# Performance work log

Hardware: AMD Instinct MI355X
Metric: run time of the kernel (lower is better)

Reference implementation:

```python
import jax, jax.numpy as jnp
import numpy as np

B, S, D = 1, 2048, 2048
H, KV, HD = 16, 2, 128        # heads, kv heads, head_dim
Q_SIZE, KV_SIZE = H * HD, KV * HD
NEG = -1e9


def setup_inputs() -> dict:
    key = jax.random.key(0)
    ks = jax.random.split(key, 5)
    hidden_states = jax.random.normal(ks[0], (B, S, D), dtype=jnp.float32)
    # rotary tables (Gemma/Qwen style: theta=10000, half-dim frequencies)
    inv_freq = 1.0 / (10000.0 ** (jnp.arange(0, HD, 2, dtype=jnp.float32) / HD))  # [HD/2]
    angles = jnp.arange(S, dtype=jnp.float32)[:, None] * inv_freq[None, :]        # [S, HD/2]
    freqs_cos = jnp.cos(angles)
    freqs_sin = jnp.sin(angles)
    kv_write_indices = jnp.arange(S, dtype=jnp.int32)
    k_cache = jnp.zeros((B, S, KV, HD), dtype=jnp.float32)
    v_cache = jnp.zeros((B, S, KV, HD), dtype=jnp.float32)
    causal = jnp.tril(jnp.ones((S, S), dtype=bool))
    mask = jnp.where(causal, 0.0, NEG).astype(jnp.float32)[None, None]  # [1,1,S,S]
    W_qkv = jax.random.normal(ks[1], (D, Q_SIZE + 2 * KV_SIZE), dtype=jnp.float32) * (D ** -0.5)
    b_qkv = jax.random.normal(ks[2], (Q_SIZE + 2 * KV_SIZE,), dtype=jnp.float32) * 0.02
    W_o = jax.random.normal(ks[3], (Q_SIZE, D), dtype=jnp.float32) * (Q_SIZE ** -0.5)
    return {
        "hidden_states": hidden_states, "freqs_cos": freqs_cos, "freqs_sin": freqs_sin,
        "kv_write_indices": kv_write_indices, "k_cache": k_cache, "v_cache": v_cache,
        "mask": mask, "W_qkv": W_qkv, "b_qkv": b_qkv, "W_o": W_o,
    }


def _rope(x, cos, sin):
    # x: [B, S, h, HD]; cos/sin: [S, HD/2]. Half-split (Gemma complex) layout.
    x1, x2 = jnp.split(x, 2, axis=-1)
    c = cos[None, :, None, :]
    s = sin[None, :, None, :]
    return jnp.concatenate([x1 * c - x2 * s, x1 * s + x2 * c], axis=-1)


def reference(hidden_states, freqs_cos, freqs_sin, kv_write_indices,
              k_cache, v_cache, mask, W_qkv, b_qkv, W_o):
    b, s, _ = hidden_states.shape
    qkv = hidden_states @ W_qkv + b_qkv                       # [B,S,(H+2KV)*HD]
    xq, xk, xv = jnp.split(qkv, [Q_SIZE, Q_SIZE + KV_SIZE], axis=-1)
    xq = xq.reshape(b, s, H, HD)
    xk = xk.reshape(b, s, KV, HD)
    xv = xv.reshape(b, s, KV, HD)
    xq = _rope(xq, freqs_cos, freqs_sin)
    xk = _rope(xk, freqs_cos, freqs_sin)
    # KV-cache write (index_copy_ along seq dim)
    key = k_cache.at[:, kv_write_indices].set(xk)             # [B,T,KV,HD]
    value = v_cache.at[:, kv_write_indices].set(xv)
    # GQA: repeat_interleave kv heads to H
    nrep = H // KV
    key = jnp.repeat(key, nrep, axis=2)                       # [B,T,H,HD]
    value = jnp.repeat(value, nrep, axis=2)
    q = jnp.transpose(xq, (0, 2, 1, 3)) * (HD ** -0.5)        # [B,H,S,HD]
    k = jnp.transpose(key, (0, 2, 1, 3))                      # [B,H,T,HD]
    v = jnp.transpose(value, (0, 2, 1, 3))
    scores = jnp.einsum("bhqd,bhkd->bhqk", q, k) + mask       # [B,H,S,T]
    probs = jax.nn.softmax(scores, axis=-1)
    out = jnp.einsum("bhqk,bhkd->bhqd", probs, v)             # [B,H,S,HD]
    out = jnp.transpose(out, (0, 2, 1, 3)).reshape(b, s, Q_SIZE)
    return out @ W_o                                          # [B,S,D]
```

## Files before the change

kernel.cpp:

```cpp
#include <hip/hip_runtime.h>
#include <hip/hip_bf16.h>

#define S_LEN 2048
#define D_MODEL 2048
#define NH 16
#define NKV 2
#define HD 128
#define QKV_N 2560
#define Q_SCALE_L2E (0.08838834764831845f * 1.4426950408889634f)

#define EPP 192

typedef short short8 __attribute__((ext_vector_type(8)));
typedef short s16x4 __attribute__((ext_vector_type(4)));
typedef float f32x4 __attribute__((ext_vector_type(4)));
using u16 = unsigned short;

struct PartTab {
  int ent[EPP];
  int rpStart[64];
  int rpN[64];
  constexpr PartTab() : ent{}, rpStart{}, rpN{} {
    int T[64] = {}, n[64] = {};
    int S = 0;
    for (int rp = 0; rp < 64; ++rp) {
      T[rp] = (rp + 2) >> 1;
      n[rp] = (T[rp] + 5) / 6;
      S += n[rp];
    }
    while (S > EPP) {
      int best = -1, bc = 1 << 30;
      for (int rp = 0; rp < 64; ++rp)
        if (n[rp] > 1) {
          int c = (T[rp] + n[rp] - 2) / (n[rp] - 1);
          if (c < bc) { bc = c; best = rp; }
        }
      --n[best]; --S;
    }
    int e = 0;
    for (int rp = 0; rp < 64; ++rp) {
      rpStart[rp] = e;
      rpN[rp] = n[rp];
      for (int c = 0; c < n[rp]; ++c) {
        int tlo = c * T[rp] / n[rp];
        int thi = (c + 1) * T[rp] / n[rp];
        ent[e++] = rp | (tlo << 6) | ((thi - tlo) << 12) | ((n[rp] == 1) ? (1 << 18) : 0);
      }
    }
  }
};
__constant__ PartTab d_tab = PartTab();

__device__ inline u16 f2b(float x) {
  __hip_bfloat16 h = __float2bfloat16(x);
  return *(u16*)&h;
}
__device__ inline float b2f(u16 x) {
  __hip_bfloat16 h = *(__hip_bfloat16*)&x;
  return __bfloat162float(h);
}
__device__ inline bool is_f32(const unsigned int* fc) {
  return (fc[0] & 0xFFFFu) == 0u;
}
__device__ inline u16 ld_cvt(const void* p, size_t i, bool f32) {
  return f32 ? f2b(((const float*)p)[i]) : ((const u16*)p)[i];
}

__device__ inline void async_copy16(const u16* g, u16* l) {
  __builtin_amdgcn_global_load_lds(
      (const __attribute__((address_space(1))) unsigned int*)g,
      (__attribute__((address_space(3))) unsigned int*)l, 16, 0, 0);
}

__global__ void convert_k(const void* __restrict__ in, u16* __restrict__ out,
                          int n, const unsigned int* __restrict__ fc) {
  const bool f32 = is_f32(fc);
  int i = blockIdx.x * 256 + threadIdx.x;
  if (i < n) out[i] = ld_cvt(in, i, f32);
}

__global__ void prep_k(const void* __restrict__ fcos, const void* __restrict__ fsin,
                       const void* __restrict__ bqkv, u16* __restrict__ cCos,
                       u16* __restrict__ cSin, u16* __restrict__ cBias) {
  const bool f32 = is_f32((const unsigned int*)fcos);
  int i = blockIdx.x * 256 + threadIdx.x;
  if (i < 131072)       cCos[i] = ld_cvt(fcos, i, f32);
  else if (i < 262144)  cSin[i - 131072] = ld_cvt(fsin, i - 131072, f32);
  else if (i < 264704)  cBias[i - 262144] = ld_cvt(bqkv, i - 262144, f32);
}

__global__ void transpose_k(const void* __restrict__ in, u16* __restrict__ out,
                            int R, int C, const unsigned int* __restrict__ fc) {
  __shared__ u16 tile[64][65];
  const bool f32 = is_f32(fc);
  const int t = threadIdx.x;
  const int r0 = blockIdx.y * 64, c0 = blockIdx.x * 64;
  for (int i = 0; i < 16; ++i) {
    int idx = i * 256 + t;
    int r = idx >> 6, c = idx & 63;
    tile[r][c] = ld_cvt(in, (size_t)(r0 + r) * C + c0 + c, f32);
  }
  __syncthreads();
  for (int i = 0; i < 16; ++i) {
    int idx = i * 256 + t;
    int r = idx >> 6, c = idx & 63;
    out[(size_t)(c0 + r) * R + r0 + c] = tile[c][r];
  }
}

template<int M, int N, int K, int KS>
__global__ __launch_bounds__(256, 2) void gemm_splitk(const u16* __restrict__ A,
                                                      const u16* __restrict__ BT,
                                                      u16* __restrict__ P0,
                                                      u16* __restrict__ P1) {
  __shared__ __align__(16) u16 lA[16 * 64 * 8];
  __shared__ __align__(16) u16 lB[16 * 64 * 8];
  const int t = threadIdx.x, lane = t & 63, w = t >> 6;
  const int wr = w & 1, wc = w >> 1;
  const int m0 = blockIdx.y * 128, n0 = blockIdx.x * 128;
  const int koff = blockIdx.z * KS;
  const int l15 = lane & 15, quad = lane >> 4;
  const int swz = (quad * 16 + (l15 ^ quad)) * 8;

  int srcoff[4], sdst[4];
  for (int qq = 0; qq < 4; ++qq) {
    int f = qq * 256 + t;
    int row = f >> 3, kc = f & 7;
    int j = kc >> 2, q4 = kc & 3, tile = row >> 4, lr = row & 15;
    sdst[qq] = ((j * 8 + tile) * 64 + q4 * 16 + (lr ^ q4)) * 8;
    srcoff[qq] = row * K + kc * 8;
  }

  f32x4 acc[4][4] = {};
  for (int k0 = koff; k0 < koff + KS; k0 += 64) {
    short8 av[4], bv[4];
    for (int qq = 0; qq < 4; ++qq) {
      av[qq] = *(const short8*)&A [(size_t)m0 * K + k0 + srcoff[qq]];
      bv[qq] = *(const short8*)&BT[(size_t)n0 * K + k0 + srcoff[qq]];
    }
    __syncthreads();
    for (int qq = 0; qq < 4; ++qq) {
      *(short8*)&lA[sdst[qq]] = av[qq];
      *(short8*)&lB[sdst[qq]] = bv[qq];
    }
    __syncthreads();
    for (int j = 0; j < 2; ++j) {
      short8 af[4], bf[4];
      for (int i = 0; i < 4; ++i)
        af[i] = *(const short8*)&lA[(j * 8 + wr * 4 + i) * 512 + swz];
      for (int jj = 0; jj < 4; ++jj)
        bf[jj] = *(const short8*)&lB[(j * 8 + wc * 4 + jj) * 512 + swz];
      for (int i = 0; i < 4; ++i)
        for (int jj = 0; jj < 4; ++jj)
          acc[i][jj] = __builtin_amdgcn_mfma_f32_16x16x32_bf16(af[i], bf[jj],
                                                               acc[i][jj], 0, 0, 0);
    }
  }

  u16* P = blockIdx.z ? P1 : P0;
  for (int i = 0; i < 4; ++i)
    for (int jj = 0; jj < 4; ++jj) {
      int row = m0 + wr * 64 + i * 16 + quad * 4;
      int col = n0 + wc * 64 + jj * 16 + l15;
      for (int r = 0; r < 4; ++r)
        P[(size_t)(row + r) * N + col] = f2b(acc[i][jj][r]);
    }
}


__global__ void rope_k(const u16* __restrict__ P0, const u16* __restrict__ P1,
                       const u16* __restrict__ bias, const u16* __restrict__ cosT,
                       const u16* __restrict__ sinT, const int* __restrict__ idx,
                       u16* __restrict__ q, u16* __restrict__ kfrag) {
  const int s = blockIdx.y;
  const int c = blockIdx.x * 256 + threadIdx.x;
  const bool isq = c < 2048;
  int d, colbase;
  if (isq) { d = c & 127; colbase = c & ~127; }
  else     { int c2 = c - 2048; d = c2 & 127; colbase = 2048 + (c2 & ~127); }
  const int dd = d & 63;
  const size_t b1 = (size_t)s * QKV_N + colbase + dd;
  float x1 = b2f(P0[b1]) + b2f(P1[b1]) + b2f(bias[colbase + dd]);
  float x2 = b2f(P0[b1 + 64]) + b2f(P1[b1 + 64]) + b2f(bias[colbase + dd + 64]);
  float cv = b2f(cosT[s * 64 + dd]);
  float sv = b2f(sinT[s * 64 + dd]);
  float v = (d < 64) ? (x1 * cv - x2 * sv) : (x1 * sv + x2 * cv);
  if (isq) {
    q[(size_t)s * D_MODEL + c] = f2b(v * Q_SCALE_L2E);
  } else {
    int c2 = c - 2048;
    int kvh = c2 >> 7, dcol = c2 & 127;
    int srow = idx[s];
    int sblk = srow >> 6, ns = (srow >> 4) & 3, lr = srow & 15;
    int cc = dcol >> 5, qd = (dcol >> 3) & 3, j = dcol & 7;
    kfrag[kvh * 262144 + sblk * 8192 + ((ns * 4 + cc) * 64 + qd * 16 + lr) * 8 + j] = f2b(v);
  }
}

__global__ void vscat_k(const u16* __restrict__ P0, const u16* __restrict__ P1,
                        const u16* __restrict__ bias, const int* __restrict__ idx,
                        u16* __restrict__ vfrag) {
  int id = blockIdx.x * 256 + threadIdx.x;
  int s = id >> 8, cv = id & 255;
  int kvh = cv >> 7, dcol = cv & 127;
  const size_t gi = (size_t)s * QKV_N + 2304 + cv;
  float v = b2f(P0[gi]) + b2f(P1[gi]) + b2f(bias[2304 + cv]);
  int srow = idx[s];
  int sblk = srow >> 6, kvl = srow & 63;
  int c2 = kvl >> 5, qd = (kvl >> 2) & 3, j = ((kvl >> 4) & 1) * 4 + (kvl & 3);
  int d = dcol >> 4, lr = dcol & 15;
  vfrag[kvh * 262144 + sblk * 8192 + ((c2 * 8 + d) * 64 + qd * 16 + lr) * 8 + j] = f2b(v);
}

__global__ void reduce_out_k(const u16* __restrict__ G0, const u16* __restrict__ G1,
                             void* __restrict__ out, const unsigned int* __restrict__ fc) {
  const bool f32 = is_f32(fc);
  int i = blockIdx.x * 256 + threadIdx.x;
  float v = b2f(G0[i]) + b2f(G1[i]);
  if (f32) ((float*)out)[i] = v;
  else     ((u16*)out)[i] = f2b(v);
}

__global__ __launch_bounds__(256, 3) void attn_part_k(const u16* __restrict__ Q,
                                                      const u16* __restrict__ Kf,
                                                      const u16* __restrict__ Vf,
                                                      u16* __restrict__ attnOut,
                                                      u16* __restrict__ pO_A,
                                                      u16* __restrict__ pO_B,
                                                      float* __restrict__ ml) {
  __shared__ __align__(16) u16 sm[16384];
  const int t = threadIdx.x, lane = t & 63, w = t >> 6;
  const int l15 = lane & 15, quad = lane >> 4;

  const int b = blockIdx.x;
  const int plane = b / EPP;
  const int ent = d_tab.ent[b - plane * EPP];
  const int rp = ent & 63, tlo = (ent >> 6) & 63, nkb = (ent >> 12) & 63;
  const bool direct = (ent >> 18) & 1;
  const int kvh = plane >> 1, hh = plane & 1;
  const int h = kvh * 8 + hh * 4 + w;
  const int qrow0 = rp * 32;
  const int kv_lo = tlo * 64;
  const int gw = b * 4 + w;

  const u16* Kb = Kf + kvh * 262144;
  const u16* Vb = Vf + kvh * 262144;

  short8 aq[2][4];
  for (int ss = 0; ss < 2; ++ss)
    for (int cc = 0; cc < 4; ++cc)
      aq[ss][cc] = *(const short8*)&Q[(size_t)(qrow0 + ss * 16 + l15) * D_MODEL
                                      + h * HD + cc * 32 + quad * 8];

  f32x4 oacc[2][8] = {};
  float m_i[2] = {-1e30f, -1e30f}, l_i[2] = {0.0f, 0.0f};

  {
    const u16* kt = Kb + (size_t)(kv_lo >> 6) * 8192;
    const u16* vt = Vb + (size_t)(kv_lo >> 6) * 8192;
    for (int f = 0; f < 4; ++f) {
      int fr = w * 4 + f;
      async_copy16(kt + fr * 512 + lane * 8, &sm[fr * 512]);
      async_copy16(vt + fr * 512 + lane * 8, &sm[8192 + fr * 512]);
    }
  }
  __syncthreads();

  for (int kb = 0; kb < nkb; ++kb) {
    const int kv0 = kv_lo + kb * 64;
    f32x4 st[2][4] = {};
    __builtin_amdgcn_s_setprio(1);
    for (int ns = 0; ns < 4; ++ns) {
      short8 bk[4];
      for (int cc = 0; cc < 4; ++cc)
        bk[cc] = *(const short8*)&sm[((ns * 4 + cc) * 64 + lane) * 8];
      for (int ss = 0; ss < 2; ++ss)
        for (int cc = 0; cc < 4; ++cc)
          st[ss][ns] = __builtin_amdgcn_mfma_f32_16x16x32_bf16(bk[cc], aq[ss][cc],
                                                               st[ss][ns], 0, 0, 0);
    }
    __builtin_amdgcn_s_setprio(0);
    __syncthreads();
    if (kb + 1 < nkb) {
      const u16* kt = Kb + (size_t)((kv0 + 64) >> 6) * 8192;
      for (int f = 0; f < 4; ++f) {
        int fr = w * 4 + f;
        async_copy16(kt + fr * 512 + lane * 8, &sm[fr * 512]);
      }
    }
    const bool need_mask = (kv0 + 63) > qrow0;
    short8 pb[2][2];
    for (int ss = 0; ss < 2; ++ss) {
      float mb = -1e30f;
      if (need_mask) {
        int qg = qrow0 + ss * 16 + l15;
        #pragma unroll
        for (int ns = 0; ns < 4; ++ns) {
          int kvg = kv0 + ns * 16 + quad * 4;
          #pragma unroll
          for (int rr = 0; rr < 4; ++rr) {
            float s = (kvg + rr <= qg) ? st[ss][ns][rr] : -1e30f;
            st[ss][ns][rr] = s;
            mb = fmaxf(mb, s);
          }
        }
      } else {
        #pragma unroll
        for (int ns = 0; ns < 4; ++ns)
          #pragma unroll
          for (int rr = 0; rr < 4; ++rr) mb = fmaxf(mb, st[ss][ns][rr]);
      }
      mb = fmaxf(mb, __shfl_xor(mb, 16, 64));
      mb = fmaxf(mb, __shfl_xor(mb, 32, 64));
      if (!__all(mb <= m_i[ss] + 8.0f)) {
        float mn = fmaxf(m_i[ss], mb);
        float alpha = exp2f(m_i[ss] - mn);
        m_i[ss] = mn;
        l_i[ss] *= alpha;
        #pragma unroll
        for (int dt = 0; dt < 8; ++dt) oacc[ss][dt] *= alpha;
      }
      float rs = 0.0f;
      #pragma unroll
      for (int ns = 0; ns < 4; ++ns)
        #pragma unroll
        for (int rr = 0; rr < 4; ++rr) {
          float e = exp2f(st[ss][ns][rr] - m_i[ss]);
          rs += e;
          pb[ss][ns >> 1][(ns & 1) * 4 + rr] = (short)f2b(e);
        }
      rs += __shfl_xor(rs, 16, 64);
      rs += __shfl_xor(rs, 32, 64);
      l_i[ss] += rs;
    }
    __builtin_amdgcn_s_setprio(1);
    for (int c2 = 0; c2 < 2; ++c2)
      for (int dt = 0; dt < 8; ++dt) {
        short8 av = *(const short8*)&sm[8192 + ((c2 * 8 + dt) * 64 + lane) * 8];
        for (int ss = 0; ss < 2; ++ss)
          oacc[ss][dt] = __builtin_amdgcn_mfma_f32_16x16x32_bf16(av, pb[ss][c2],
                                                                 oacc[ss][dt], 0, 0, 0);
      }
    __builtin_amdgcn_s_setprio(0);
    if (kb + 1 < nkb) {
      __syncthreads();
      const u16* vt = Vb + (size_t)((kv0 + 64) >> 6) * 8192;
      for (int f = 0; f < 4; ++f) {
        int fr = w * 4 + f;
        async_copy16(vt + fr * 512 + lane * 8, &sm[8192 + fr * 512]);
      }
    }
  }

  __syncthreads();
  u16* Ow = &sm[w * 2176];
  const int er = lane >> 2, ec = lane & 3;
  for (int ss = 0; ss < 2; ++ss) {
    float inv = direct ? (1.0f / l_i[ss]) : 1.0f;
    for (int dt = 0; dt < 8; ++dt) {
      s16x4 pk;
      for (int rr = 0; rr < 4; ++rr) pk[rr] = (short)f2b(oacc[ss][dt][rr] * inv);
      *(s16x4*)&Ow[l15 * 136 + dt * 16 + quad * 4] = pk;
    }
    __builtin_amdgcn_s_waitcnt(0xC07F);
    short8 o0 = *(const short8*)&Ow[er * 136 + ec * 32];
    short8 o1 = *(const short8*)&Ow[er * 136 + ec * 32 + 8];
    short8 o2 = *(const short8*)&Ow[er * 136 + ec * 32 + 16];
    short8 o3 = *(const short8*)&Ow[er * 136 + ec * 32 + 24];
    __builtin_amdgcn_s_waitcnt(0xC07F);
    if (direct) {
      size_t ga = (size_t)(qrow0 + ss * 16 + er) * D_MODEL + h * HD + ec * 32;
      *(short8*)&attnOut[ga]      = o0;
      *(short8*)&attnOut[ga + 8]  = o1;
      *(short8*)&attnOut[ga + 16] = o2;
      *(short8*)&attnOut[ga + 24] = o3;
    } else {
      u16* po = (gw < 2048) ? (pO_A + (size_t)gw * 4096)
                            : (pO_B + (size_t)(gw - 2048) * 4096);
      int ra = (ss * 16 + er) * 128 + ec * 32;
      *(short8*)&po[ra]      = o0;
      *(short8*)&po[ra + 8]  = o1;
      *(short8*)&po[ra + 16] = o2;
      *(short8*)&po[ra + 24] = o3;
      if (quad == 0) {
        ml[gw * 64 + (ss * 16 + l15) * 2]     = m_i[ss];
        ml[gw * 64 + (ss * 16 + l15) * 2 + 1] = l_i[ss];
      }
    }
  }
}

__global__ void attn_combine_k(const u16* __restrict__ pO_A,
                               const u16* __restrict__ pO_B,
                               const float* __restrict__ ml,
                               u16* __restrict__ attn) {
  const int h = blockIdx.x >> 6, rp = blockIdx.x & 63;
  const int nch = d_tab.rpN[rp];
  if (nch == 1) return;
  const int start = d_tab.rpStart[rp];
  const int t = threadIdx.x;
  const int row = t >> 3;
  const int dblk = t & 7;
  const int plane = (h >> 3) * 2 + ((h >> 2) & 1);
  const int w = h & 3;

  int gws[8];
  float wt[8];
  float mx = -1e30f;
  for (int c = 0; c < nch; ++c) {
    gws[c] = (plane * EPP + start + c) * 4 + w;
    mx = fmaxf(mx, ml[gws[c] * 64 + row * 2]);
  }
  float lsum = 0.0f;
  for (int c = 0; c < nch; ++c) {
    float m = ml[gws[c] * 64 + row * 2];
    float l = ml[gws[c] * 64 + row * 2 + 1];
    wt[c] = exp2f(m - mx);
    lsum += l * wt[c];
  }
  float inv = 1.0f / lsum;

  float acc[16];
  #pragma unroll
  for (int j = 0; j < 16; ++j) acc[j] = 0.0f;
  const int poff = row * 128 + dblk * 16;
  for (int c = 0; c < nch; ++c) {
    const u16* po = (gws[c] < 2048) ? (pO_A + (size_t)gws[c] * 4096)
                                    : (pO_B + (size_t)(gws[c] - 2048) * 4096);
    short8 lo = *(const short8*)&po[poff];
    short8 hi = *(const short8*)&po[poff + 8];
    float wc = wt[c];
    #pragma unroll
    for (int j = 0; j < 8; ++j) acc[j]     += b2f((u16)lo[j]) * wc;
    #pragma unroll
    for (int j = 0; j < 8; ++j) acc[8 + j] += b2f((u16)hi[j]) * wc;
  }
  short8 o0, o1;
  #pragma unroll
  for (int j = 0; j < 8; ++j) o0[j] = (short)f2b(acc[j] * inv);
  #pragma unroll
  for (int j = 0; j < 8; ++j) o1[j] = (short)f2b(acc[8 + j] * inv);
  const size_t orow = (size_t)(rp * 32 + row) * D_MODEL + h * HD + dblk * 16;
  *(short8*)&attn[orow]     = o0;
  *(short8*)&attn[orow + 8] = o1;
}

extern "C" void kernel_launch(void* const* d_in, const int* in_sizes, int n_in,
                              void* d_out, int out_size, void* d_ws, size_t ws_size,
                              hipStream_t stream) {
  const void* hidden = d_in[0];
  const void* fcos   = d_in[1];
  const void* fsin   = d_in[2];
  const int* idx     = (const int*)d_in[3];
  u16* maskScratch   = (u16*)d_in[6];
  const void* Wqkv = d_in[7];
  const void* bqkv = d_in[8];
  const void* Wo   = d_in[9];
  const unsigned int* fc = (const unsigned int*)fcos;

  u16* ws = (u16*)d_ws;
  u16* cHid   = ws;
  u16* cCos   = ws + 4194304;
  u16* cSin   = ws + 4325376;
  u16* cBias  = ws + 4456448;
  u16* WqkvT  = ws + 4461056;
  u16* q      = WqkvT;
  u16* G1     = WqkvT;
  u16* P0     = ws + 9703936;
  u16* attn   = P0;
  u16* P1     = ws + 14946816;
  u16* pO_B   = P1;
  float* ml   = (float*)(P1 + 4194304);
  u16* WoT    = ws + 20189696;
  u16* kfrag  = ws;
  u16* vfrag  = ws + 524288;
  u16* G0     = ws;

  convert_k<<<(4194304 + 255) / 256, 256, 0, stream>>>(hidden, cHid, 4194304, fc);
  prep_k<<<(264704 + 255) / 256, 256, 0, stream>>>(fcos, fsin, bqkv, cCos, cSin, cBias);
  transpose_k<<<dim3(40, 32), 256, 0, stream>>>(Wqkv, WqkvT, D_MODEL, QKV_N, fc);
  transpose_k<<<dim3(32, 32), 256, 0, stream>>>(Wo, WoT, D_MODEL, D_MODEL, fc);
  gemm_splitk<S_LEN, QKV_N, D_MODEL, D_MODEL / 2>
      <<<dim3(QKV_N / 128, S_LEN / 128, 2), 256, 0, stream>>>(cHid, WqkvT, P0, P1);
  rope_k<<<dim3(9, S_LEN), 256, 0, stream>>>(P0, P1, cBias, cCos, cSin, idx, q, kfrag);
  vscat_k<<<2048, 256, 0, stream>>>(P0, P1, cBias, idx, vfrag);
  attn_part_k<<<4 * EPP, 256, 0, stream>>>(q, kfrag, vfrag, attn, maskScratch, pO_B, ml);
  attn_combine_k<<<16 * 64, 256, 0, stream>>>(maskScratch, pO_B, ml, attn);
  gemm_splitk<S_LEN, D_MODEL, D_MODEL, D_MODEL / 2>
      <<<dim3(D_MODEL / 128, S_LEN / 128, 2), 256, 0, stream>>>(attn, WoT, G0, G1);
  reduce_out_k<<<4194304 / 256, 256, 0, stream>>>(G0, G1, d_out, fc);
}
```

Before: 260.2 us.

## Vectorize elementwise kernels, fuse rope with V scatter, double-buffer attention K/V

Converts the convert, prep, transpose and reduce kernels to 8- or 4-wide vector loads and stores, replacing per-element accesses. Merges the rope and V-scatter kernels into one launch, with each rope thread now computing both halves of a rotation pair. Double-buffers K and V tiles in LDS within the attention kernel, prefetching the next block at the top of each iteration and dropping one barrier per step. The larger LDS footprint lowers the launch bound from 3 to 2 blocks per CU, which may reduce occupancy.

```diff
diff --git a/kernel.cpp b/kernel.cpp
--- a/kernel.cpp
+++ b/kernel.cpp
@@ -65,6 +65,19 @@
 __device__ inline u16 ld_cvt(const void* p, size_t i, bool f32) {
   return f32 ? f2b(((const float*)p)[i]) : ((const u16*)p)[i];
 }
+__device__ inline short8 ld8_cvt(const void* p, size_t i8, bool f32) {
+  short8 o;
+  if (f32) {
+    const float* f = (const float*)p + i8 * 8;
+    f32x4 a = *(const f32x4*)f;
+    f32x4 b = *(const f32x4*)(f + 4);
+    #pragma unroll
+    for (int j = 0; j < 4; ++j) { o[j] = (short)f2b(a[j]); o[4 + j] = (short)f2b(b[j]); }
+  } else {
+    o = *(const short8*)((const u16*)p + i8 * 8);
+  }
+  return o;
+}
 
 __device__ inline void async_copy16(const u16* g, u16* l) {
   __builtin_amdgcn_global_load_lds(
@@ -73,10 +86,10 @@
 }
 
 __global__ void convert_k(const void* __restrict__ in, u16* __restrict__ out,
-                          int n, const unsigned int* __restrict__ fc) {
+                          int n8, const unsigned int* __restrict__ fc) {
   const bool f32 = is_f32(fc);
   int i = blockIdx.x * 256 + threadIdx.x;
-  if (i < n) out[i] = ld_cvt(in, i, f32);
+  if (i < n8) *(short8*)&out[(size_t)i * 8] = ld8_cvt(in, i, f32);
 }
 
 __global__ void prep_k(const void* __restrict__ fcos, const void* __restrict__ fsin,
@@ -84,9 +97,9 @@
                        u16* __restrict__ cSin, u16* __restrict__ cBias) {
   const bool f32 = is_f32((const unsigned int*)fcos);
   int i = blockIdx.x * 256 + threadIdx.x;
-  if (i < 131072)       cCos[i] = ld_cvt(fcos, i, f32);
-  else if (i < 262144)  cSin[i - 131072] = ld_cvt(fsin, i - 131072, f32);
-  else if (i < 264704)  cBias[i - 262144] = ld_cvt(bqkv, i - 262144, f32);
+  if (i < 16384)       *(short8*)&cCos[(size_t)i * 8] = ld8_cvt(fcos, i, f32);
+  else if (i < 32768)  *(short8*)&cSin[(size_t)(i - 16384) * 8] = ld8_cvt(fsin, i - 16384, f32);
+  else if (i < 33088)  *(short8*)&cBias[(size_t)(i - 32768) * 8] = ld8_cvt(bqkv, i - 32768, f32);
 }
 
 __global__ void transpose_k(const void* __restrict__ in, u16* __restrict__ out,
@@ -95,16 +108,27 @@
   const bool f32 = is_f32(fc);
   const int t = threadIdx.x;
   const int r0 = blockIdx.y * 64, c0 = blockIdx.x * 64;
-  for (int i = 0; i < 16; ++i) {
-    int idx = i * 256 + t;
+  for (int i = 0; i < 4; ++i) {
+    int idx = (i * 256 + t) * 4;
     int r = idx >> 6, c = idx & 63;
-    tile[r][c] = ld_cvt(in, (size_t)(r0 + r) * C + c0 + c, f32);
+    if (f32) {
+      f32x4 v = *(const f32x4*)&((const float*)in)[(size_t)(r0 + r) * C + c0 + c];
+      #pragma unroll
+      for (int j = 0; j < 4; ++j) tile[r][c + j] = f2b(v[j]);
+    } else {
+      s16x4 v = *(const s16x4*)&((const u16*)in)[(size_t)(r0 + r) * C + c0 + c];
+      #pragma unroll
+      for (int j = 0; j < 4; ++j) tile[r][c + j] = (u16)v[j];
+    }
   }
   __syncthreads();
-  for (int i = 0; i < 16; ++i) {
-    int idx = i * 256 + t;
+  for (int i = 0; i < 4; ++i) {
+    int idx = (i * 256 + t) * 4;
     int r = idx >> 6, c = idx & 63;
-    out[(size_t)(c0 + r) * R + r0 + c] = tile[c][r];
+    s16x4 o;
+    #pragma unroll
+    for (int j = 0; j < 4; ++j) o[j] = (short)tile[c + j][r];
+    *(s16x4*)&out[(size_t)(c0 + r) * R + r0 + c] = o;
   }
 }
 
@@ -168,67 +192,82 @@
 }
 
 
-__global__ void rope_k(const u16* __restrict__ P0, const u16* __restrict__ P1,
-                       const u16* __restrict__ bias, const u16* __restrict__ cosT,
-                       const u16* __restrict__ sinT, const int* __restrict__ idx,
-                       u16* __restrict__ q, u16* __restrict__ kfrag) {
+__global__ void ropev_k(const u16* __restrict__ P0, const u16* __restrict__ P1,
+                        const u16* __restrict__ bias, const u16* __restrict__ cosT,
+                        const u16* __restrict__ sinT, const int* __restrict__ idx,
+                        u16* __restrict__ q, u16* __restrict__ kfrag,
+                        u16* __restrict__ vfrag) {
   const int s = blockIdx.y;
-  const int c = blockIdx.x * 256 + threadIdx.x;
-  const bool isq = c < 2048;
-  int d, colbase;
-  if (isq) { d = c & 127; colbase = c & ~127; }
-  else     { int c2 = c - 2048; d = c2 & 127; colbase = 2048 + (c2 & ~127); }
-  const int dd = d & 63;
-  const size_t b1 = (size_t)s * QKV_N + colbase + dd;
-  float x1 = b2f(P0[b1]) + b2f(P1[b1]) + b2f(bias[colbase + dd]);
-  float x2 = b2f(P0[b1 + 64]) + b2f(P1[b1 + 64]) + b2f(bias[colbase + dd + 64]);
-  float cv = b2f(cosT[s * 64 + dd]);
-  float sv = b2f(sinT[s * 64 + dd]);
-  float v = (d < 64) ? (x1 * cv - x2 * sv) : (x1 * sv + x2 * cv);
-  if (isq) {
-    q[(size_t)s * D_MODEL + c] = f2b(v * Q_SCALE_L2E);
+  const int id = blockIdx.x * 256 + threadIdx.x;
+  if (id >= 1408) return;
+  if (id < 1152) {
+    const int colbase = (id < 1024) ? (id >> 6) * 128
+                                    : 2048 + ((id - 1024) >> 6) * 128;
+    const int dd = id & 63;
+    const size_t b1 = (size_t)s * QKV_N + colbase + dd;
+    float x1 = b2f(P0[b1]) + b2f(P1[b1]) + b2f(bias[colbase + dd]);
+    float x2 = b2f(P0[b1 + 64]) + b2f(P1[b1 + 64]) + b2f(bias[colbase + dd + 64]);
+    float cv = b2f(cosT[s * 64 + dd]);
+    float sv = b2f(sinT[s * 64 + dd]);
+    float o1 = x1 * cv - x2 * sv;
+    float o2 = x1 * sv + x2 * cv;
+    if (id < 1024) {
+      q[(size_t)s * D_MODEL + colbase + dd]      = f2b(o1 * Q_SCALE_L2E);
+      q[(size_t)s * D_MODEL + colbase + dd + 64] = f2b(o2 * Q_SCALE_L2E);
+    } else {
+      int kvh = (colbase - 2048) >> 7;
+      int srow = idx[s];
+      int sblk = srow >> 6, ns = (srow >> 4) & 3, lr = srow & 15;
+      int cc1 = dd >> 5, qd1 = (dd >> 3) & 3, j1 = dd & 7;
+      kfrag[kvh * 262144 + sblk * 8192 + ((ns * 4 + cc1) * 64 + qd1 * 16 + lr) * 8 + j1] = f2b(o1);
+      int d2 = dd + 64;
+      int cc2 = d2 >> 5, qd2 = (d2 >> 3) & 3, j2 = d2 & 7;
+      kfrag[kvh * 262144 + sblk * 8192 + ((ns * 4 + cc2) * 64 + qd2 * 16 + lr) * 8 + j2] = f2b(o2);
+    }
   } else {
-    int c2 = c - 2048;
-    int kvh = c2 >> 7, dcol = c2 & 127;
+    const int cv_ = id - 1152;
+    const int kvh = cv_ >> 7, dcol = cv_ & 127;
+    const size_t gi = (size_t)s * QKV_N + 2304 + cv_;
+    float v = b2f(P0[gi]) + b2f(P1[gi]) + b2f(bias[2304 + cv_]);
     int srow = idx[s];
-    int sblk = srow >> 6, ns = (srow >> 4) & 3, lr = srow & 15;
-    int cc = dcol >> 5, qd = (dcol >> 3) & 3, j = dcol & 7;
-    kfrag[kvh * 262144 + sblk * 8192 + ((ns * 4 + cc) * 64 + qd * 16 + lr) * 8 + j] = f2b(v);
-  }
-}
-
-__global__ void vscat_k(const u16* __restrict__ P0, const u16* __restrict__ P1,
-                        const u16* __restrict__ bias, const int* __restrict__ idx,
-                        u16* __restrict__ vfrag) {
-  int id = blockIdx.x * 256 + threadIdx.x;
-  int s = id >> 8, cv = id & 255;
-  int kvh = cv >> 7, dcol = cv & 127;
-  const size_t gi = (size_t)s * QKV_N + 2304 + cv;
-  float v = b2f(P0[gi]) + b2f(P1[gi]) + b2f(bias[2304 + cv]);
-  int srow = idx[s];
-  int sblk = srow >> 6, kvl = srow & 63;
-  int c2 = kvl >> 5, qd = (kvl >> 2) & 3, j = ((kvl >> 4) & 1) * 4 + (kvl & 3);
-  int d = dcol >> 4, lr = dcol & 15;
-  vfrag[kvh * 262144 + sblk * 8192 + ((c2 * 8 + d) * 64 + qd * 16 + lr) * 8 + j] = f2b(v);
+    int sblk = srow >> 6, kvl = srow & 63;
+    int c2 = kvl >> 5, qd = (kvl >> 2) & 3, j = ((kvl >> 4) & 1) * 4 + (kvl & 3);
+    int d = dcol >> 4, lr = dcol & 15;
+    vfrag[kvh * 262144 + sblk * 8192 + ((c2 * 8 + d) * 64 + qd * 16 + lr) * 8 + j] = f2b(v);
+  }
 }
 
 __global__ void reduce_out_k(const u16* __restrict__ G0, const u16* __restrict__ G1,
                              void* __restrict__ out, const unsigned int* __restrict__ fc) {
   const bool f32 = is_f32(fc);
   int i = blockIdx.x * 256 + threadIdx.x;
-  float v = b2f(G0[i]) + b2f(G1[i]);
-  if (f32) ((float*)out)[i] = v;
-  else     ((u16*)out)[i] = f2b(v);
-}
-
-__global__ __launch_bounds__(256, 3) void attn_part_k(const u16* __restrict__ Q,
+  short8 a = *(const short8*)&G0[(size_t)i * 8];
+  short8 b = *(const short8*)&G1[(size_t)i * 8];
+  if (f32) {
+    f32x4 lo, hi;
+    #pragma unroll
+    for (int j = 0; j < 4; ++j) {
+      lo[j] = b2f((u16)a[j]) + b2f((u16)b[j]);
+      hi[j] = b2f((u16)a[4 + j]) + b2f((u16)b[4 + j]);
+    }
+    ((f32x4*)out)[(size_t)i * 2]     = lo;
+    ((f32x4*)out)[(size_t)i * 2 + 1] = hi;
+  } else {
+    short8 o;
+    #pragma unroll
+    for (int j = 0; j < 8; ++j) o[j] = (short)f2b(b2f((u16)a[j]) + b2f((u16)b[j]));
+    ((short8*)out)[i] = o;
+  }
+}
+
+__global__ __launch_bounds__(256, 2) void attn_part_k(const u16* __restrict__ Q,
                                                       const u16* __restrict__ Kf,
                                                       const u16* __restrict__ Vf,
                                                       u16* __restrict__ attnOut,
                                                       u16* __restrict__ pO_A,
                                                       u16* __restrict__ pO_B,
                                                       float* __restrict__ ml) {
-  __shared__ __align__(16) u16 sm[16384];
+  __shared__ __align__(16) u16 sm[32768];
   const int t = threadIdx.x, lane = t & 63, w = t >> 6;
   const int l15 = lane & 15, quad = lane >> 4;
 
@@ -268,26 +307,29 @@
 
   for (int kb = 0; kb < nkb; ++kb) {
     const int kv0 = kv_lo + kb * 64;
+    const int cur = (kb & 1) * 16384;
+    const int nxt = cur ^ 16384;
+    if (kb + 1 < nkb) {
+      const u16* kt = Kb + (size_t)((kv0 + 64) >> 6) * 8192;
+      const u16* vt = Vb + (size_t)((kv0 + 64) >> 6) * 8192;
+      for (int f = 0; f < 4; ++f) {
+        int fr = w * 4 + f;
+        async_copy16(kt + fr * 512 + lane * 8, &sm[nxt + fr * 512]);
+        async_copy16(vt + fr * 512 + lane * 8, &sm[nxt + 8192 + fr * 512]);
+      }
+    }
     f32x4 st[2][4] = {};
     __builtin_amdgcn_s_setprio(1);
     for (int ns = 0; ns < 4; ++ns) {
       short8 bk[4];
       for (int cc = 0; cc < 4; ++cc)
-        bk[cc] = *(const short8*)&sm[((ns * 4 + cc) * 64 + lane) * 8];
+        bk[cc] = *(const short8*)&sm[cur + ((ns * 4 + cc) * 64 + lane) * 8];
       for (int ss = 0; ss < 2; ++ss)
         for (int cc = 0; cc < 4; ++cc)
           st[ss][ns] = __builtin_amdgcn_mfma_f32_16x16x32_bf16(bk[cc], aq[ss][cc],
                                                                st[ss][ns], 0, 0, 0);
     }
     __builtin_amdgcn_s_setprio(0);
-    __syncthreads();
-    if (kb + 1 < nkb) {
-      const u16* kt = Kb + (size_t)((kv0 + 64) >> 6) * 8192;
-      for (int f = 0; f < 4; ++f) {
-        int fr = w * 4 + f;
-        async_copy16(kt + fr * 512 + lane * 8, &sm[fr * 512]);
-      }
-    }
     const bool need_mask = (kv0 + 63) > qrow0;
     short8 pb[2][2];
     for (int ss = 0; ss < 2; ++ss) {
@@ -336,23 +378,15 @@
     __builtin_amdgcn_s_setprio(1);
     for (int c2 = 0; c2 < 2; ++c2)
       for (int dt = 0; dt < 8; ++dt) {
-        short8 av = *(const short8*)&sm[8192 + ((c2 * 8 + dt) * 64 + lane) * 8];
+        short8 av = *(const short8*)&sm[cur + 8192 + ((c2 * 8 + dt) * 64 + lane) * 8];
         for (int ss = 0; ss < 2; ++ss)
           oacc[ss][dt] = __builtin_amdgcn_mfma_f32_16x16x32_bf16(av, pb[ss][c2],
                                                                  oacc[ss][dt], 0, 0, 0);
       }
     __builtin_amdgcn_s_setprio(0);
-    if (kb + 1 < nkb) {
-      __syncthreads();
-      const u16* vt = Vb + (size_t)((kv0 + 64) >> 6) * 8192;
-      for (int f = 0; f < 4; ++f) {
-        int fr = w * 4 + f;
-        async_copy16(vt + fr * 512 + lane * 8, &sm[8192 + fr * 512]);
-      }
-    }
-  }
-
-  __syncthreads();
+    __syncthreads();
+  }
+
   u16* Ow = &sm[w * 2176];
   const int er = lane >> 2, ec = lane & 3;
   for (int ss = 0; ss < 2; ++ss) {
@@ -476,17 +510,16 @@
   u16* vfrag  = ws + 524288;
   u16* G0     = ws;
 
-  convert_k<<<(4194304 + 255) / 256, 256, 0, stream>>>(hidden, cHid, 4194304, fc);
-  prep_k<<<(264704 + 255) / 256, 256, 0, stream>>>(fcos, fsin, bqkv, cCos, cSin, cBias);
+  convert_k<<<2048, 256, 0, stream>>>(hidden, cHid, 524288, fc);
+  prep_k<<<130, 256, 0, stream>>>(fcos, fsin, bqkv, cCos, cSin, cBias);
   transpose_k<<<dim3(40, 32), 256, 0, stream>>>(Wqkv, WqkvT, D_MODEL, QKV_N, fc);
   transpose_k<<<dim3(32, 32), 256, 0, stream>>>(Wo, WoT, D_MODEL, D_MODEL, fc);
   gemm_splitk<S_LEN, QKV_N, D_MODEL, D_MODEL / 2>
       <<<dim3(QKV_N / 128, S_LEN / 128, 2), 256, 0, stream>>>(cHid, WqkvT, P0, P1);
-  rope_k<<<dim3(9, S_LEN), 256, 0, stream>>>(P0, P1, cBias, cCos, cSin, idx, q, kfrag);
-  vscat_k<<<2048, 256, 0, stream>>>(P0, P1, cBias, idx, vfrag);
+  ropev_k<<<dim3(6, S_LEN), 256, 0, stream>>>(P0, P1, cBias, cCos, cSin, idx, q, kfrag, vfrag);
   attn_part_k<<<4 * EPP, 256, 0, stream>>>(q, kfrag, vfrag, attn, maskScratch, pO_B, ml);
   attn_combine_k<<<16 * 64, 256, 0, stream>>>(maskScratch, pO_B, ml, attn);
   gemm_splitk<S_LEN, D_MODEL, D_MODEL, D_MODEL / 2>
       <<<dim3(D_MODEL / 128, S_LEN / 128, 2), 256, 0, stream>>>(attn, WoT, G0, G1);
-  reduce_out_k<<<4194304 / 256, 256, 0, stream>>>(G0, G1, d_out, fc);
-}
+  reduce_out_k<<<2048, 256, 0, stream>>>(G0, G1, d_out, fc);
+}
```

Result: faster. 248.8 us (-4.4%).
